# Kernel optimization log

Measured on AMD Instinct MI355X. Metric: run time of the kernel, lower is better.

Reference implementation:

```python
import jax, jax.numpy as jnp
import numpy as np

TOP_K = 2
EPS = 1e-9

def setup_inputs() -> dict:
    key = jax.random.key(0)
    ks = jax.random.split(key, 8)
    B, L, C, F = 64, 512, 3, 300          # batteries, cycles, channels, curve length
    d_model, d_llm, d_ff, E = 512, 4096, 2048, 8
    s = lambda k, sh: jax.random.normal(k, sh, jnp.float32) * 0.02
    return dict(
        cycle_curve_data=jax.random.normal(ks[0], (B, L, C, F), jnp.float32),
        cycle_numbers=jax.random.uniform(ks[1], (B, 1), jnp.float32),
        DKP_embeddings=jax.random.normal(ks[2], (B, d_llm), jnp.float32),
        gate_W1=s(ks[3], (d_llm + 1, d_ff)), gate_b1=jnp.zeros((d_ff,), jnp.float32),
        gate_W2=s(ks[4], (d_ff, E)), gate_b2=jnp.zeros((E,), jnp.float32),
        expert_W=s(ks[5], (E, C * F, d_model)), expert_b=jnp.zeros((E, d_model), jnp.float32),
        gen_W=s(ks[6], (C * F, d_model)), gen_b=jnp.zeros((d_model,), jnp.float32),
    )

def reference(cycle_curve_data, cycle_numbers, DKP_embeddings,
              gate_W1, gate_b1, gate_W2, gate_b2,
              expert_W, expert_b, gen_W, gen_b):
    B, L, C, F = cycle_curve_data.shape
    # router (PatternRouter_two): 2-layer MLP over [DKP embedding ; cycle number]
    g_in = jnp.concatenate([DKP_embeddings, cycle_numbers], axis=-1)   # [B, d_llm+1]
    h = jax.nn.gelu(g_in @ gate_W1 + gate_b1)
    logits = h @ gate_W2 + gate_b2                                     # [B, E]
    # top-k mask on raw logits (as in source), softmax, mask, renormalize
    _, idx = jax.lax.top_k(logits, TOP_K)
    mask = jnp.zeros(logits.shape, bool).at[jnp.arange(B)[:, None], idx].set(True)
    p = jax.nn.softmax(logits, axis=1)
    g = jnp.where(mask, p, 0.0)
    gates = g / (jnp.sum(g, axis=1, keepdims=True) + EPS)              # [B, E]
    # experts: flatten(start_dim=2) then Linear(3*F -> d_model); combine is linear
    # so fold gates into a per-battery weight: sum_e gates[b,e] * W_e
    x = cycle_curve_data.reshape(B, L, C * F)                          # [B, L, 3F]
    Wb = jnp.einsum('be,eid->bid', gates, expert_W)                    # [B, 3F, d]
    bb = gates @ expert_b                                              # [B, d]
    moe_out = jnp.einsum('bli,bid->bld', x, Wb) + bb[:, None, :]       # [B, L, d]
    general = x @ gen_W + gen_b                                        # [B, L, d]
    # source casts the combined MoE output to bf16 before adding
    return general + moe_out.astype(jnp.bfloat16)
```

## Files before the change

kernel.cpp:

```cpp
#include <hip/hip_runtime.h>
#include <hip/hip_bf16.h>
#include <stdint.h>

typedef __attribute__((ext_vector_type(8))) short short8;
typedef __attribute__((ext_vector_type(4))) short short4v;
typedef __attribute__((ext_vector_type(4))) float f32x4;

__device__ inline unsigned short f2bf(float f) {
    union { float f; uint32_t u; } v; v.f = f;
    uint32_t u = v.u;
    uint32_t r = (u + 0x7FFFu + ((u >> 16) & 1u)) >> 16;
    return (unsigned short)r;
}

__device__ inline short4v pk4(float4 a) {
    short4v r;
    r[0] = (short)f2bf(a.x); r[1] = (short)f2bf(a.y);
    r[2] = (short)f2bf(a.z); r[3] = (short)f2bf(a.w);
    return r;
}

__global__ __launch_bounds__(256) void router1(const float* __restrict__ DKP,
                                               const float* __restrict__ W1,
                                               float* __restrict__ part) {
    __shared__ float gin[16 * 64];
    const int t  = threadIdx.x;
    const int bg = blockIdx.x & 3, jc = blockIdx.x >> 2;
    const int ks = blockIdx.y;
    const int k0 = ks * 64;
    {
        const int b = t >> 4, q = t & 15;
        *(float4*)(gin + b * 64 + q * 4) =
            *(const float4*)(DKP + (size_t)(bg * 16 + b) * 4096 + k0 + q * 4);
    }
    __syncthreads();
    const int ja = jc * 512 + t, jb = ja + 256;
    float accA[16], accB[16];
    #pragma unroll
    for (int b = 0; b < 16; ++b) { accA[b] = 0.f; accB[b] = 0.f; }
    #pragma unroll 1
    for (int oct = 0; oct < 8; ++oct) {
        const int kk = oct * 8;
        float wa[8], wb[8];
        #pragma unroll
        for (int i = 0; i < 8; ++i) {
            const float* wr = W1 + (size_t)(k0 + kk + i) * 2048;
            wa[i] = wr[ja]; wb[i] = wr[jb];
        }
        #pragma unroll
        for (int b = 0; b < 16; ++b) {
            float4 g0 = *(const float4*)(gin + b * 64 + kk);
            float4 g1 = *(const float4*)(gin + b * 64 + kk + 4);
            accA[b] += g0.x*wa[0] + g0.y*wa[1] + g0.z*wa[2] + g0.w*wa[3]
                     + g1.x*wa[4] + g1.y*wa[5] + g1.z*wa[6] + g1.w*wa[7];
            accB[b] += g0.x*wb[0] + g0.y*wb[1] + g0.z*wb[2] + g0.w*wb[3]
                     + g1.x*wb[4] + g1.y*wb[5] + g1.z*wb[6] + g1.w*wb[7];
        }
    }
    #pragma unroll 1
    for (int b = 0; b < 16; ++b) {
        const size_t row = (size_t)(ks * 64 + bg * 16 + b) * 2048;
        part[row + ja] = accA[b];
        part[row + jb] = accB[b];
    }
}

__global__ __launch_bounds__(256) void router2(const float* __restrict__ part,
                                               const float* __restrict__ cyc,
                                               const float* __restrict__ W1,
                                               const float* __restrict__ b1,
                                               float* __restrict__ h) {
    const int idx = blockIdx.x * 256 + threadIdx.x;
    const int j = idx & 2047, b = idx >> 11;
    float s = 0.f;
    #pragma unroll 8
    for (int t = 0; t < 64; ++t)
        s += part[((size_t)t * 64 + b) * 2048 + j];
    s += cyc[b] * W1[(size_t)4096 * 2048 + j] + b1[j];
    const float u  = s + 0.044715f * s * s * s;
    const float th = tanhf(0.7978845608028654f * u);
    h[idx] = 0.5f * s * (1.0f + th);
}

__global__ __launch_bounds__(256) void router3(const float* __restrict__ h,
                                               const float* __restrict__ W2,
                                               const float* __restrict__ b2,
                                               float4* __restrict__ gates) {
    __shared__ float red[256 * 8];
    __shared__ float lg[8];
    const int b = blockIdx.x, t = threadIdx.x;
    float acc[8];
    #pragma unroll
    for (int e = 0; e < 8; ++e) acc[e] = 0.f;
    for (int k = t; k < 2048; k += 256) {
        const float hv = h[(size_t)b * 2048 + k];
        const float* w = W2 + (size_t)k * 8;
        #pragma unroll
        for (int e = 0; e < 8; ++e) acc[e] += hv * w[e];
    }
    #pragma unroll
    for (int e = 0; e < 8; ++e) red[t * 8 + e] = acc[e];
    __syncthreads();
    if (t < 8) {
        float s = 0.f;
        for (int r = 0; r < 256; ++r) s += red[r * 8 + t];
        lg[t] = s + b2[t];
    }
    __syncthreads();
    if (t == 0) {
        float l[8];
        #pragma unroll
        for (int e = 0; e < 8; ++e) l[e] = lg[e];
        int e0 = 0;
        #pragma unroll
        for (int e = 1; e < 8; ++e) if (l[e] > l[e0]) e0 = e;
        int e1 = (e0 == 0) ? 1 : 0;
        #pragma unroll
        for (int e = 0; e < 8; ++e) if (e != e0 && l[e] > l[e1]) e1 = e;
        const float m = l[e0];
        float p[8], Z = 0.f;
        #pragma unroll
        for (int e = 0; e < 8; ++e) { p[e] = expf(l[e] - m); Z += p[e]; }
        const float pe0 = p[e0] / Z, pe1 = p[e1] / Z;
        const float s2 = pe0 + pe1 + 1e-9f;
        gates[b] = make_float4(__int_as_float(e0), __int_as_float(e1), pe0 / s2, pe1 / s2);
    }
}

__global__ __launch_bounds__(256) void combine_w(const float* __restrict__ genW,
                                                 const float* __restrict__ expW,
                                                 const float4* __restrict__ gates,
                                                 unsigned short* __restrict__ wc) {
    __shared__ unsigned short T[64 * 72];
    const int b  = blockIdx.z;
    const int i0 = blockIdx.y * 64;
    const int d0 = blockIdx.x * 64;
    const float4 gt = gates[b];
    const int e0 = __float_as_int(gt.x), e1 = __float_as_int(gt.y);
    const float g0 = gt.z, g1 = gt.w;
    const float* W0 = expW + (size_t)e0 * 900 * 512;
    const float* W1e = expW + (size_t)e1 * 900 * 512;
    const int t = threadIdx.x;
    {
        const int il = t >> 2, c = t & 3;
        const int i = i0 + il;
        const bool valid = (i < 900);
        const size_t rowoff = (size_t)i * 512 + d0 + c * 16;
        #pragma unroll
        for (int s = 0; s < 4; ++s) {
            float4 g  = valid ? *(const float4*)(genW + rowoff + 4 * s) : make_float4(0,0,0,0);
            float4 w0 = valid ? *(const float4*)(W0   + rowoff + 4 * s) : make_float4(0,0,0,0);
            float4 w1 = valid ? *(const float4*)(W1e  + rowoff + 4 * s) : make_float4(0,0,0,0);
            const int dl = c * 16 + 4 * s;
            T[(dl + 0) * 72 + il] = f2bf(g.x + g0 * w0.x + g1 * w1.x);
            T[(dl + 1) * 72 + il] = f2bf(g.y + g0 * w0.y + g1 * w1.y);
            T[(dl + 2) * 72 + il] = f2bf(g.z + g0 * w0.z + g1 * w1.z);
            T[(dl + 3) * 72 + il] = f2bf(g.w + g0 * w0.w + g1 * w1.w);
        }
    }
    __syncthreads();
    {
        const int dl = t >> 2, seg = t & 3;
        const int ic = seg * 16;
        if (i0 + ic < 928) {
            short8 v0 = *(const short8*)&T[dl * 72 + ic];
            short8 v1 = *(const short8*)&T[dl * 72 + ic + 8];
            unsigned short* dst = wc + (size_t)b * 512 * 928 + (size_t)(d0 + dl) * 928 + i0 + ic;
            *(short8*)dst = v0;
            *((short8*)dst + 1) = v1;
        }
    }
}

__global__ __launch_bounds__(512, 4) void moe_gemm(const float* __restrict__ x,
                                                   const unsigned short* __restrict__ wc,
                                                   const float4* __restrict__ gates,
                                                   const float* __restrict__ eb,
                                                   const float* __restrict__ genb,
                                                   float* __restrict__ out) {
    __shared__ unsigned short As[64 * 40];
    __shared__ unsigned short Bs[512 * 32];
    const int b  = blockIdx.x;
    const int m0 = blockIdx.y * 64;
    const int t = threadIdx.x, lane = t & 63, wid = t >> 6;
    const float4 gt = gates[b];
    const int e0 = __float_as_int(gt.x), e1 = __float_as_int(gt.y);
    const float g0 = gt.z, g1 = gt.w;
    const float* xb = x + (size_t)b * 512 * 900;
    const unsigned short* wcb = wc + (size_t)b * 512 * 928;
    f32x4 acc[4][4];
    #pragma unroll
    for (int mi = 0; mi < 4; ++mi)
        #pragma unroll
        for (int ni = 0; ni < 4; ++ni)
            acc[mi][ni] = (f32x4){0.f, 0.f, 0.f, 0.f};

    const int arow  = t >> 3;
    const int akoff = (t & 7) * 4;
    const float* xrow = xb + (size_t)(m0 + arow) * 900 + akoff;
    const int bseg = (lane & 3) ^ ((lane >> 3) & 3);
    const int burow = lane >> 2;

    const int wn = wid * 64;
    const int lm = lane & 15, lq = lane >> 4;

    for (int kt = 0; kt < 29; ++kt) {
        const int k0 = kt * 32;
        #pragma unroll
        for (int r = 0; r < 4; ++r) {
            const int chunk = wid * 4 + r;
            const int n = chunk * 16 + burow;
            const unsigned short* gsrc = wcb + (size_t)n * 928 + k0 + bseg * 8;
            unsigned short* ldst = &Bs[chunk * 512];
            __builtin_amdgcn_global_load_lds(
                (const __attribute__((address_space(1))) unsigned int*)gsrc,
                (__attribute__((address_space(3))) unsigned int*)ldst, 16, 0, 0);
        }
        float4 f;
        if (k0 + 32 <= 900) {
            f = *(const float4*)(xrow + k0);
        } else {
            float v[4];
            #pragma unroll
            for (int i = 0; i < 4; ++i) {
                const int k = k0 + akoff + i;
                v[i] = (k < 900) ? xrow[k0 + i] : 0.f;
            }
            f = make_float4(v[0], v[1], v[2], v[3]);
        }
        *(short4v*)&As[arow * 40 + akoff] = pk4(f);
        __syncthreads();
        short8 af[4], bf[4];
        #pragma unroll
        for (int mi = 0; mi < 4; ++mi)
            af[mi] = *(const short8*)&As[(mi * 16 + lm) * 40 + lq * 8];
        #pragma unroll
        for (int ni = 0; ni < 4; ++ni) {
            const int n = wn + ni * 16 + lm;
            const int slot = lq ^ ((lm >> 1) & 3);
            bf[ni] = *(const short8*)&Bs[n * 32 + slot * 8];
        }
        #pragma unroll
        for (int mi = 0; mi < 4; ++mi)
            #pragma unroll
            for (int ni = 0; ni < 4; ++ni)
                acc[mi][ni] = __builtin_amdgcn_mfma_f32_16x16x32_bf16(
                    af[mi], bf[ni], acc[mi][ni], 0, 0, 0);
        __syncthreads();
    }
    #pragma unroll
    for (int ni = 0; ni < 4; ++ni) {
        const int col = wn + ni * 16 + lm;
        const float bias = genb[col] + g0 * eb[e0 * 512 + col] + g1 * eb[e1 * 512 + col];
        #pragma unroll
        for (int mi = 0; mi < 4; ++mi) {
            const int row = m0 + mi * 16 + lq * 4;
            #pragma unroll
            for (int r = 0; r < 4; ++r)
                out[((size_t)b * 512 + row + r) * 512 + col] = acc[mi][ni][r] + bias;
        }
    }
}

extern "C" void kernel_launch(void* const* d_in, const int* in_sizes, int n_in,
                              void* d_out, int out_size, void* d_ws, size_t ws_size,
                              hipStream_t stream) {
    const float* x    = (const float*)d_in[0];
    const float* cyc  = (const float*)d_in[1];
    const float* dkp  = (const float*)d_in[2];
    const float* gW1  = (const float*)d_in[3];
    const float* gb1  = (const float*)d_in[4];
    const float* gW2  = (const float*)d_in[5];
    const float* gb2  = (const float*)d_in[6];
    const float* eW   = (const float*)d_in[7];
    const float* eb   = (const float*)d_in[8];
    const float* genW = (const float*)d_in[9];
    const float* genb = (const float*)d_in[10];
    float* out = (float*)d_out;

    char* ws = (char*)d_ws;
    unsigned short* wcomb = (unsigned short*)ws;
    float* part  = (float*)ws;
    float* h     = (float*)(ws + 60817408);
    float4* gts  = (float4*)(ws + 60817408 + 524288);

    router1<<<dim3(16, 64), 256, 0, stream>>>(dkp, gW1, part);
    router2<<<512, 256, 0, stream>>>(part, cyc, gW1, gb1, h);
    router3<<<64, 256, 0, stream>>>(h, gW2, gb2, gts);
    combine_w<<<dim3(8, 15, 64), 256, 0, stream>>>(genW, eW, gts, wcomb);
    moe_gemm<<<dim3(64, 8), 512, 0, stream>>>(x, wcomb, gts, eb, genb, out);
}
```

Measured before the change: 400.0 us.

## Retile MoE GEMM to 128x128 blocks with double-buffered LDS prefetch

After: 438.0 us. +9.5%, slower.

```diff
diff --git a/kernel.cpp b/kernel.cpp
--- a/kernel.cpp
+++ b/kernel.cpp
@@ -172,22 +172,24 @@
     }
 }
 
-__global__ __launch_bounds__(512, 4) void moe_gemm(const float* __restrict__ x,
+__global__ __launch_bounds__(256, 4) void moe_gemm(const float* __restrict__ x,
                                                    const unsigned short* __restrict__ wc,
                                                    const float4* __restrict__ gates,
                                                    const float* __restrict__ eb,
                                                    const float* __restrict__ genb,
                                                    float* __restrict__ out) {
-    __shared__ unsigned short As[64 * 40];
-    __shared__ unsigned short Bs[512 * 32];
-    const int b  = blockIdx.x;
-    const int m0 = blockIdx.y * 64;
+    __shared__ unsigned short As[2][128 * 32];
+    __shared__ unsigned short Bs[2][128 * 32];
+    const int b    = blockIdx.x;
+    const int tile = blockIdx.y;
+    const int m0 = (tile >> 2) * 128, n0 = (tile & 3) * 128;
     const int t = threadIdx.x, lane = t & 63, wid = t >> 6;
     const float4 gt = gates[b];
     const int e0 = __float_as_int(gt.x), e1 = __float_as_int(gt.y);
     const float g0 = gt.z, g1 = gt.w;
     const float* xb = x + (size_t)b * 512 * 900;
     const unsigned short* wcb = wc + (size_t)b * 512 * 928;
+
     f32x4 acc[4][4];
     #pragma unroll
     for (int mi = 0; mi < 4; ++mi)
@@ -195,71 +197,89 @@
         for (int ni = 0; ni < 4; ++ni)
             acc[mi][ni] = (f32x4){0.f, 0.f, 0.f, 0.f};
 
-    const int arow  = t >> 3;
-    const int akoff = (t & 7) * 4;
-    const float* xrow = xb + (size_t)(m0 + arow) * 900 + akoff;
-    const int bseg = (lane & 3) ^ ((lane >> 3) & 3);
-    const int burow = lane >> 2;
-
-    const int wn = wid * 64;
+    const int ar = t >> 1, ah = t & 1;
+    const float* xrow = xb + (size_t)(m0 + ar) * 900 + ah * 16;
+    const int fa = (ar >> 1) & 3;
+    const int bu = lane >> 2, bsl = lane & 3;
+    const int bseg = bsl ^ ((bu >> 1) & 3);
+
+    const int wm = (wid >> 1) * 64, wn = (wid & 1) * 64;
     const int lm = lane & 15, lq = lane >> 4;
-
+    const int fslot = (lq ^ ((lm >> 1) & 3)) * 8;
+
+    float4 apf[4];
+
+    #define LOAD_A(K0)                                                          \
+        {   const int _k0 = (K0);                                               \
+            _Pragma("unroll")                                                   \
+            for (int q = 0; q < 4; ++q) {                                       \
+                const int k = _k0 + ah * 16 + q * 4;                            \
+                apf[q] = (k + 4 <= 900) ? *(const float4*)(xrow + _k0 + q * 4)  \
+                                        : make_float4(0.f, 0.f, 0.f, 0.f);      \
+            }                                                                   \
+        }
+    #define WRITE_A(BUF)                                                        \
+        {   _Pragma("unroll")                                                   \
+            for (int q = 0; q < 4; ++q) {                                       \
+                const int koff = ah * 16 + q * 4;                               \
+                const int sl = (koff >> 3) ^ fa;                                \
+                *(short4v*)&As[BUF][ar * 32 + sl * 8 + (koff & 7)] = pk4(apf[q]); \
+            }                                                                   \
+        }
+    #define STAGE_B(K0, BUF)                                                    \
+        {   const int _k0 = (K0);                                               \
+            _Pragma("unroll")                                                   \
+            for (int r2 = 0; r2 < 2; ++r2) {                                    \
+                const int chunk = wid * 2 + r2;                                 \
+                const unsigned short* gsrc =                                    \
+                    wcb + (size_t)(n0 + chunk * 16 + bu) * 928 + _k0 + bseg * 8;\
+                __builtin_amdgcn_global_load_lds(                               \
+                    (const __attribute__((address_space(1))) unsigned int*)gsrc,\
+                    (__attribute__((address_space(3))) unsigned int*)            \
+                        (&Bs[BUF][chunk * 512]), 16, 0, 0);                     \
+            }                                                                   \
+        }
+
+    LOAD_A(0); STAGE_B(0, 0); WRITE_A(0);
+    __syncthreads();
+
+    int cur = 0;
     for (int kt = 0; kt < 29; ++kt) {
-        const int k0 = kt * 32;
-        #pragma unroll
-        for (int r = 0; r < 4; ++r) {
-            const int chunk = wid * 4 + r;
-            const int n = chunk * 16 + burow;
-            const unsigned short* gsrc = wcb + (size_t)n * 928 + k0 + bseg * 8;
-            unsigned short* ldst = &Bs[chunk * 512];
-            __builtin_amdgcn_global_load_lds(
-                (const __attribute__((address_space(1))) unsigned int*)gsrc,
-                (__attribute__((address_space(3))) unsigned int*)ldst, 16, 0, 0);
-        }
-        float4 f;
-        if (k0 + 32 <= 900) {
-            f = *(const float4*)(xrow + k0);
-        } else {
-            float v[4];
-            #pragma unroll
-            for (int i = 0; i < 4; ++i) {
-                const int k = k0 + akoff + i;
-                v[i] = (k < 900) ? xrow[k0 + i] : 0.f;
-            }
-            f = make_float4(v[0], v[1], v[2], v[3]);
-        }
-        *(short4v*)&As[arow * 40 + akoff] = pk4(f);
-        __syncthreads();
-        short8 af[4], bf[4];
+        const int nxt = cur ^ 1;
+        if (kt < 28) { LOAD_A((kt + 1) * 32); STAGE_B((kt + 1) * 32, nxt); }
+        short8 af[4], bfr[4];
         #pragma unroll
         for (int mi = 0; mi < 4; ++mi)
-            af[mi] = *(const short8*)&As[(mi * 16 + lm) * 40 + lq * 8];
-        #pragma unroll
-        for (int ni = 0; ni < 4; ++ni) {
-            const int n = wn + ni * 16 + lm;
-            const int slot = lq ^ ((lm >> 1) & 3);
-            bf[ni] = *(const short8*)&Bs[n * 32 + slot * 8];
-        }
+            af[mi] = *(const short8*)&As[cur][(wm + mi * 16 + lm) * 32 + fslot];
+        #pragma unroll
+        for (int ni = 0; ni < 4; ++ni)
+            bfr[ni] = *(const short8*)&Bs[cur][(wn + ni * 16 + lm) * 32 + fslot];
         #pragma unroll
         for (int mi = 0; mi < 4; ++mi)
             #pragma unroll
             for (int ni = 0; ni < 4; ++ni)
                 acc[mi][ni] = __builtin_amdgcn_mfma_f32_16x16x32_bf16(
-                    af[mi], bf[ni], acc[mi][ni], 0, 0, 0);
+                    af[mi], bfr[ni], acc[mi][ni], 0, 0, 0);
+        if (kt < 28) WRITE_A(nxt);
         __syncthreads();
-    }
+        cur = nxt;
+    }
+
     #pragma unroll
     for (int ni = 0; ni < 4; ++ni) {
-        const int col = wn + ni * 16 + lm;
+        const int col = n0 + wn + ni * 16 + lm;
         const float bias = genb[col] + g0 * eb[e0 * 512 + col] + g1 * eb[e1 * 512 + col];
         #pragma unroll
         for (int mi = 0; mi < 4; ++mi) {
-            const int row = m0 + mi * 16 + lq * 4;
+            const int row = m0 + wm + mi * 16 + lq * 4;
             #pragma unroll
             for (int r = 0; r < 4; ++r)
                 out[((size_t)b * 512 + row + r) * 512 + col] = acc[mi][ni][r] + bias;
         }
     }
+    #undef LOAD_A
+    #undef WRITE_A
+    #undef STAGE_B
 }
 
 extern "C" void kernel_launch(void* const* d_in, const int* in_sizes, int n_in,
@@ -288,5 +308,5 @@
     router2<<<512, 256, 0, stream>>>(part, cyc, gW1, gb1, h);
     router3<<<64, 256, 0, stream>>>(h, gW2, gb2, gts);
     combine_w<<<dim3(8, 15, 64), 256, 0, stream>>>(genW, eW, gts, wcomb);
-    moe_gemm<<<dim3(64, 8), 512, 0, stream>>>(x, wcomb, gts, eb, genb, out);
-}
+    moe_gemm<<<dim3(64, 16), 256, 0, stream>>>(x, wcomb, gts, eb, genb, out);
+}
```
